# Kernel optimization log

Measured on AMD Instinct MI355X. Metric: run time of the kernel, lower is better.

The kernel has to match this reference:

```python
import jax, jax.numpy as jnp
import numpy as np
from jax import lax

K = 7            # cfg.network.PSROI_BINS == pool_size
FEAT_STRIDE = 16
LAMDA = 0.1
D_PER_BIN = 8    # feature channels per position-sensitive bin -> C = K*K*8 = 392


def _bilinear(feat, y, x, extra_idx):
    """Bilinearly sample feat[H,W,...] at float coords (y,x); extra_idx are
    integer index arrays (broadcast to y.shape) selecting trailing feat axes."""
    H, W = feat.shape[0], feat.shape[1]
    y0f = jnp.floor(y); x0f = jnp.floor(x)
    wy = (y - y0f)[..., None]
    wx = (x - x0f)[..., None]
    y0 = jnp.clip(y0f.astype(jnp.int32), 0, H - 1)
    y1 = jnp.clip(y0f.astype(jnp.int32) + 1, 0, H - 1)
    x0 = jnp.clip(x0f.astype(jnp.int32), 0, W - 1)
    x1 = jnp.clip(x0f.astype(jnp.int32) + 1, 0, W - 1)
    def g(yi, xi):
        return feat[(yi, xi) + extra_idx]
    return ((1 - wy) * (1 - wx) * g(y0, x0) + (1 - wy) * wx * g(y0, x1)
            + wy * (1 - wx) * g(y1, x0) + wy * wx * g(y1, x1))


def ps_roi(f, rois, k, feat_stride, offsets=None):
    """Position-sensitive RoI pooling. f: [H,W,C] with C = k*k*D (bin-major
    channel layout). rois: [N,5] (batch, x1, y1, x2, y2) in image coords.
    offsets (optional): [N, k*k, G, 2] per-bin, per-channel-group (x,y) shifts
    in image coords. Returns [N, D, k, k]."""
    H, W, C = f.shape
    N = rois.shape[0]
    kk = k * k
    D = C // kk
    x1 = rois[:, 1] / feat_stride
    y1 = rois[:, 2] / feat_stride
    x2 = (rois[:, 3] + 1.0) / feat_stride
    y2 = (rois[:, 4] + 1.0) / feat_stride
    bw = (x2 - x1) / k  # [N]
    bh = (y2 - y1) / k
    jj = jnp.tile(jnp.arange(k, dtype=f.dtype), k)     # bin = i*k + j
    ii = jnp.repeat(jnp.arange(k, dtype=f.dtype), k)
    cx = x1[:, None] + (jj + 0.5) * bw[:, None]        # [N, kk] bin centers
    cy = y1[:, None] + (ii + 0.5) * bh[:, None]
    bins = jnp.arange(kk, dtype=jnp.int32)
    if offsets is None:
        feat = f.reshape(H, W, kk, D)
        b = jnp.broadcast_to(bins, (N, kk))
        vals = _bilinear(feat, cy, cx, (b,))           # [N, kk, D]
    else:
        G = offsets.shape[2]
        cxg = cx[:, :, None] + offsets[..., 0] / feat_stride  # [N, kk, G]
        cyg = cy[:, :, None] + offsets[..., 1] / feat_stride
        feat = f.reshape(H, W, kk, G, D // G)
        b = jnp.broadcast_to(bins[None, :, None], (N, kk, G))
        g = jnp.broadcast_to(jnp.arange(G, dtype=jnp.int32)[None, None, :], (N, kk, G))
        vals = _bilinear(feat, cyg, cxg, (b, g))       # [N, kk, G, D//G]
        vals = vals.reshape(N, kk, D)
    return jnp.transpose(vals.reshape(N, k, k, D), (0, 3, 1, 2))  # [N, D, k, k]


def setup_inputs():
    key = jax.random.key(0)
    kf, kw, k1, k2 = jax.random.split(key, 4)
    H = W = 128
    C = K * K * D_PER_BIN
    N = 2048
    features = jax.random.normal(kf, (1, H, W, C), jnp.float32)
    conv_w = jax.random.normal(kw, (3, 3, C, 2 * 4 * K * K), jnp.float32) * 0.01
    img = float(H * FEAT_STRIDE)
    xy1 = jax.random.uniform(k1, (N, 2), minval=0.0, maxval=img * 0.6)
    wh = jax.random.uniform(k2, (N, 2), minval=32.0, maxval=img * 0.4)
    xy2 = jnp.minimum(xy1 + wh, img - 1.0)
    rois = jnp.concatenate([jnp.zeros((N, 1)), xy1[:, :1], xy1[:, 1:], xy2[:, :1], xy2[:, 1:]], axis=1).astype(jnp.float32)
    return {"features": features, "rois": rois, "conv_w": conv_w}


def reference(features, rois, conv_w):
    # offset branch: 3x3 conv (no bias) -> PS-RoI pool -> scale by lamda*roi size
    offset_map = lax.conv_general_dilated(features, conv_w, (1, 1), 'SAME',
                                          dimension_numbers=('NHWC', 'HWIO', 'NHWC'))
    off = ps_roi(offset_map[0], rois, K, FEAT_STRIDE)          # [N, 8, K, K]
    N = off.shape[0]
    off = off.reshape(N, -1, 2, K, K)                          # [N, 4, 2, K, K]
    off = jnp.transpose(off, (2, 3, 4, 1, 0))                  # [2, K, K, 4, N]
    roi_w = rois[:, 3] - rois[:, 1] + 1.0
    roi_h = rois[:, 4] - rois[:, 2] + 1.0
    off = jnp.stack((off[0] * roi_w * LAMDA, off[1] * roi_h * LAMDA), axis=0)
    off = jnp.transpose(off, (4, 1, 2, 3, 0))                  # [N, K, K, 4, 2]
    off = off.reshape(N, K * K, -1, 2)                         # [N, kk, 4, 2]
    # deformable PS-RoI pooling of the features with predicted offsets
    return ps_roi(features[0], rois, K, FEAT_STRIDE, offsets=off)  # [N, 8, K, K]
```

## Files before the change

### kernel.cpp

```cpp
#include <hip/hip_runtime.h>
#include <hip/hip_cooperative_groups.h>
#include <cstddef>
#include <cstdint>

namespace cg = cooperative_groups;

#define HH    128
#define WW    128
#define CC    392
#define NPIX  (HH*WW)
#define NROI  2048
#define PSK   7
#define NBIN  49
#define LAMDA 0.1f

#define CPAD      448
#define HPAD      130
#define NPADCO    512
#define SEGSTRIDE (9*CPAD)
#define BKK       64
#define NQ        63

#define NBLK    1024
#define NTHR    256
#define GSTRIDE (NBLK*NTHR)
#define FTOT    (HPAD*HPAD*(CPAD/8))
#define WTILES  (9*14*16)
#define POOLTOT (NROI*NBIN*4)

typedef _Float16 half8   __attribute__((ext_vector_type(8)));
typedef _Float16 half2v  __attribute__((ext_vector_type(2)));
typedef float    floatx4 __attribute__((ext_vector_type(4)));

__device__ __forceinline__ void async_ld16(const _Float16* g, _Float16* l) {
  __builtin_amdgcn_global_load_lds((const __attribute__((address_space(1))) void*)g,
                                   (__attribute__((address_space(3))) void*)l,
                                   16, 0, 0);
}

__device__ __forceinline__ void prep_features(const float* __restrict__ F,
                                              _Float16* __restrict__ Fh,
                                              int gtid, int stride) {
  for (int idx = gtid; idx < FTOT; idx += stride) {
    const int p  = idx / (CPAD / 8);
    const int cgi = idx - p * (CPAD / 8);
    const int c  = cgi * 8;
    const int py = p / HPAD;
    const int px = p - py * HPAD;
    half8 h;
#pragma unroll
    for (int i = 0; i < 8; ++i) h[i] = (_Float16)0.f;
    if (py >= 1 && py <= HH && px >= 1 && px <= WW && c < CC) {
      const float* src = F + ((size_t)(py - 1) * WW + (px - 1)) * CC + c;
      const float4 v0 = *(const float4*)src;
      const float4 v1 = *(const float4*)(src + 4);
      h[0] = (_Float16)v0.x; h[1] = (_Float16)v0.y;
      h[2] = (_Float16)v0.z; h[3] = (_Float16)v0.w;
      h[4] = (_Float16)v1.x; h[5] = (_Float16)v1.y;
      h[6] = (_Float16)v1.z; h[7] = (_Float16)v1.w;
    }
    *(half8*)(Fh + (size_t)p * CPAD + c) = h;
  }
}

__device__ __forceinline__ void prep_weights(const float* __restrict__ Wt,
                                             _Float16* __restrict__ Bth,
                                             float (*tile)[33],
                                             int bid, int t, int nblocks) {
  for (int tl = bid; tl < WTILES; tl += nblocks) {
    const int seg = tl / (14 * 16);
    const int rem = tl - seg * (14 * 16);
    const int cit = rem / 16;
    const int cot = rem - cit * 16;
    const int ci0 = cit * 32, co0 = cot * 32;
    __syncthreads();
#pragma unroll
    for (int i = 0; i < 4; ++i) {
      const int idx = t + i * 256;
      const int lr = idx >> 5;
      const int lc = idx & 31;
      const int ci = ci0 + lr, co = co0 + lc;
      float v = 0.f;
      if (ci < CC && co < CC) v = Wt[((size_t)seg * CC + ci) * CC + co];
      tile[lr][lc] = v;
    }
    __syncthreads();
#pragma unroll
    for (int i = 0; i < 4; ++i) {
      const int idx = t + i * 256;
      const int lr = idx >> 5;
      const int lc = idx & 31;
      Bth[(size_t)(co0 + lr) * SEGSTRIDE + seg * CPAD + ci0 + lc] = (_Float16)tile[lc][lr];
    }
  }
}

__device__ __forceinline__ void conv_phase(const _Float16* __restrict__ Fh,
                                           const _Float16* __restrict__ Bth,
                                           _Float16* __restrict__ OM,
                                           _Float16* As, _Float16* Bs,
                                           int cb, int t) {
  const int L = t & 63;
  const int w = t >> 6;
  const int row0 = (cb & 127) * 128;
  const int col0 = (cb >> 7) * 128;

  const int srow = L >> 3;
  const int kofs = ((L & 7) ^ srow) * 8;

  const int ya = row0 >> 7;
  const int nbase = col0 + w * 32 + srow;

  const int wm = (w >> 1) * 64;
  const int wn = (w & 1) * 64;
  const int fr = L & 15;
  const int quad = L >> 4;
  const int pg0 = (quad ^ (fr & 7)) * 8;
  const int pg1 = ((4 + quad) ^ (fr & 7)) * 8;

  floatx4 acc[4][4];
#pragma unroll
  for (int i = 0; i < 4; ++i)
#pragma unroll
    for (int j = 0; j < 4; ++j) {
      floatx4 z = {0.f, 0.f, 0.f, 0.f};
      acc[i][j] = z;
    }

  for (int q = 0; q < NQ; ++q) {
    const int seg = q / 7;
    const int it  = q - seg * 7;
    const int dy = seg / 3 - 1;
    const int dx = seg - (seg / 3) * 3 - 1;
    const int fy = ya + 1 + dy;
    const int cbofs = it * BKK;
    const _Float16* gArow = Fh + ((size_t)fy * HPAD + (1 + dx)) * CPAD + kofs + cbofs;
    const _Float16* gB = Bth + (size_t)nbase * SEGSTRIDE + seg * CPAD + kofs + cbofs;

#pragma unroll
    for (int j = 0; j < 4; ++j) {
      const int xr = w * 32 + j * 8 + srow;
      async_ld16(gArow + (size_t)xr * CPAD, &As[(w * 32 + j * 8) * BKK]);
    }
#pragma unroll
    for (int j = 0; j < 4; ++j) {
      async_ld16(gB + (size_t)(j * 8) * SEGSTRIDE, &Bs[(w * 32 + j * 8) * BKK]);
    }
    __syncthreads();

    half8 a0[4], a1[4], b0[4], b1[4];
#pragma unroll
    for (int mt = 0; mt < 4; ++mt) {
      const int rb = (wm + mt * 16 + fr) * BKK;
      a0[mt] = *(const half8*)(&As[rb + pg0]);
      a1[mt] = *(const half8*)(&As[rb + pg1]);
    }
#pragma unroll
    for (int nt = 0; nt < 4; ++nt) {
      const int rb = (wn + nt * 16 + fr) * BKK;
      b0[nt] = *(const half8*)(&Bs[rb + pg0]);
      b1[nt] = *(const half8*)(&Bs[rb + pg1]);
    }
#pragma unroll
    for (int mt = 0; mt < 4; ++mt)
#pragma unroll
      for (int nt = 0; nt < 4; ++nt)
        acc[mt][nt] = __builtin_amdgcn_mfma_f32_16x16x32_f16(a0[mt], b0[nt], acc[mt][nt], 0, 0, 0);
#pragma unroll
    for (int mt = 0; mt < 4; ++mt)
#pragma unroll
      for (int nt = 0; nt < 4; ++nt)
        acc[mt][nt] = __builtin_amdgcn_mfma_f32_16x16x32_f16(a1[mt], b1[nt], acc[mt][nt], 0, 0, 0);
    __syncthreads();
  }

#pragma unroll
  for (int mt = 0; mt < 4; ++mt) {
    const int rbase = row0 + wm + mt * 16 + quad * 4;
#pragma unroll
    for (int nt = 0; nt < 4; ++nt) {
      const int col = col0 + wn + nt * 16 + fr;
      if (col < CC) {
#pragma unroll
        for (int r = 0; r < 4; ++r)
          OM[(size_t)(rbase + r) * CC + col] = (_Float16)acc[mt][nt][r];
      }
    }
  }
}

__device__ __forceinline__ void bilin_setup(float y, float x,
                                            int& iy0, int& iy1, int& ix0, int& ix1,
                                            float& w00, float& w01, float& w10, float& w11) {
  const float y0f = floorf(y), x0f = floorf(x);
  const float wy = y - y0f, wx = x - x0f;
  const int a = (int)y0f, b = (int)x0f;
  iy0 = min(max(a, 0), HH - 1);
  iy1 = min(max(a + 1, 0), HH - 1);
  ix0 = min(max(b, 0), WW - 1);
  ix1 = min(max(b + 1, 0), WW - 1);
  w00 = (1.f - wy) * (1.f - wx);
  w01 = (1.f - wy) * wx;
  w10 = wy * (1.f - wx);
  w11 = wy * wx;
}

__device__ __forceinline__ void pool_item(const _Float16* __restrict__ Fh,
                                          const float* __restrict__ R,
                                          const _Float16* __restrict__ OM,
                                          float* __restrict__ out, int tid) {
  const int g  = tid & 3;
  const int nb = tid >> 2;
  const int n  = nb / NBIN;
  const int b  = nb - n * NBIN;
  const int bi = b / PSK;
  const int bj = b - bi * PSK;

  const float rx1 = R[n * 5 + 1], ry1 = R[n * 5 + 2];
  const float rx2 = R[n * 5 + 3], ry2 = R[n * 5 + 4];
  const float x1 = rx1 * (1.f / 16.f);
  const float y1 = ry1 * (1.f / 16.f);
  const float x2 = (rx2 + 1.f) * (1.f / 16.f);
  const float y2 = (ry2 + 1.f) * (1.f / 16.f);
  const float bw = (x2 - x1) * (1.f / 7.f);
  const float bh = (y2 - y1) * (1.f / 7.f);
  const float cx = x1 + ((float)bj + 0.5f) * bw;
  const float cy = y1 + ((float)bi + 0.5f) * bh;
  const float sxs = (rx2 - rx1 + 1.f) * (LAMDA / 16.f);
  const float sys = (ry2 - ry1 + 1.f) * (LAMDA / 16.f);

  int iy0, iy1, ix0, ix1;
  float w00, w01, w10, w11;
  bilin_setup(cy, cx, iy0, iy1, ix0, ix1, w00, w01, w10, w11);

  const size_t c0 = (size_t)b * 8 + 2 * g;
  const half2v m00 = *(const half2v*)(OM + (size_t)(iy0 * WW + ix0) * CC + c0);
  const half2v m01 = *(const half2v*)(OM + (size_t)(iy0 * WW + ix1) * CC + c0);
  const half2v m10 = *(const half2v*)(OM + (size_t)(iy1 * WW + ix0) * CC + c0);
  const half2v m11 = *(const half2v*)(OM + (size_t)(iy1 * WW + ix1) * CC + c0);

  const float ox = w00 * (float)m00[0] + w01 * (float)m01[0]
                 + w10 * (float)m10[0] + w11 * (float)m11[0];
  const float oy = w00 * (float)m00[1] + w01 * (float)m01[1]
                 + w10 * (float)m10[1] + w11 * (float)m11[1];

  const float sx = cx + ox * sxs;
  const float sy = cy + oy * sys;

  int jy0, jy1, jx0, jx1;
  float u00, u01, u10, u11;
  bilin_setup(sy, sx, jy0, jy1, jx0, jx1, u00, u01, u10, u11);

  const half2v q00 = *(const half2v*)(Fh + ((size_t)(jy0 + 1) * HPAD + (jx0 + 1)) * CPAD + c0);
  const half2v q01 = *(const half2v*)(Fh + ((size_t)(jy0 + 1) * HPAD + (jx1 + 1)) * CPAD + c0);
  const half2v q10 = *(const half2v*)(Fh + ((size_t)(jy1 + 1) * HPAD + (jx0 + 1)) * CPAD + c0);
  const half2v q11 = *(const half2v*)(Fh + ((size_t)(jy1 + 1) * HPAD + (jx1 + 1)) * CPAD + c0);

  const float v0 = u00 * (float)q00[0] + u01 * (float)q01[0]
                 + u10 * (float)q10[0] + u11 * (float)q11[0];
  const float v1 = u00 * (float)q00[1] + u01 * (float)q01[1]
                 + u10 * (float)q10[1] + u11 * (float)q11[1];

  out[((size_t)n * 8 + 2 * g + 0) * NBIN + b] = v0;
  out[((size_t)n * 8 + 2 * g + 1) * NBIN + b] = v1;
}

__global__ __launch_bounds__(NTHR, 4)
void mega_kernel(const float* __restrict__ F, const float* __restrict__ R,
                 const float* __restrict__ Wt, _Float16* __restrict__ OM,
                 _Float16* __restrict__ Fh, _Float16* __restrict__ Bth,
                 float* __restrict__ out) {
  __shared__ __align__(16) _Float16 smem[2 * 128 * BKK];
  const int bid = blockIdx.x;
  const int t = threadIdx.x;
  const int gtid = bid * NTHR + t;
  cg::grid_group grid = cg::this_grid();

  prep_features(F, Fh, gtid, GSTRIDE);
  prep_weights(Wt, Bth, (float(*)[33])smem, bid, t, NBLK);

  __threadfence();
  grid.sync();

  if (bid < 512)
    conv_phase(Fh, Bth, OM, smem, smem + 128 * BKK, bid, t);

  __threadfence();
  grid.sync();

  for (int item = gtid; item < POOLTOT; item += GSTRIDE)
    pool_item(Fh, R, OM, out, item);
}

__global__ __launch_bounds__(256)
void prep_kernel_sa(const float* __restrict__ F, const float* __restrict__ Wt,
                    _Float16* __restrict__ Fh, _Float16* __restrict__ Bth) {
  __shared__ float tile[32][33];
  const int bid = blockIdx.x;
  const int t = threadIdx.x;
  prep_features(F, Fh, bid * 256 + t, gridDim.x * 256);
  prep_weights(Wt, Bth, tile, bid, t, gridDim.x);
}

__global__ __launch_bounds__(256, 4)
void conv_kernel_sa(const _Float16* __restrict__ Fh, const _Float16* __restrict__ Bth,
                    _Float16* __restrict__ OM) {
  __shared__ __align__(16) _Float16 smem[2 * 128 * BKK];
  conv_phase(Fh, Bth, OM, smem, smem + 128 * BKK, blockIdx.x, threadIdx.x);
}

__global__ __launch_bounds__(256)
void pool_kernel_sa(const _Float16* __restrict__ Fh, const float* __restrict__ R,
                    const _Float16* __restrict__ OM, float* __restrict__ out) {
  const int tid = blockIdx.x * 256 + threadIdx.x;
  if (tid < POOLTOT) pool_item(Fh, R, OM, out, tid);
}

extern "C" void kernel_launch(void* const* d_in, const int* in_sizes, int n_in,
                              void* d_out, int out_size, void* d_ws, size_t ws_size,
                              hipStream_t stream) {
  const float* F  = (const float*)d_in[0];
  const float* R  = (const float*)d_in[1];
  const float* Wt = (const float*)d_in[2];
  float* out = (float*)d_out;

  const size_t omBytes  = (size_t)NPIX * CC * sizeof(_Float16);
  const size_t fhBytes  = (size_t)HPAD * HPAD * CPAD * sizeof(_Float16);

  _Float16* OM  = (_Float16*)d_ws;
  _Float16* Fh  = (_Float16*)((char*)d_ws + omBytes);
  _Float16* Bth = (_Float16*)((char*)d_ws + omBytes + fhBytes);

  int maxBlk = 0;
  hipError_t qerr = hipOccupancyMaxActiveBlocksPerMultiprocessor(&maxBlk, mega_kernel, NTHR, 0);
  bool tryCoop = (qerr == hipSuccess && maxBlk >= 4);

  if (tryCoop) {
    void* args[] = {(void*)&F, (void*)&R, (void*)&Wt, (void*)&OM,
                    (void*)&Fh, (void*)&Bth, (void*)&out};
    hipError_t err = hipLaunchCooperativeKernel((const void*)mega_kernel,
                                                dim3(NBLK), dim3(NTHR),
                                                args, 0, stream);
    if (err == hipSuccess) return;
    (void)hipGetLastError();
  }

  prep_kernel_sa<<<2048, 256, 0, stream>>>(F, Wt, Fh, Bth);
  conv_kernel_sa<<<512, 256, 0, stream>>>(Fh, Bth, OM);
  pool_kernel_sa<<<(POOLTOT + 255) / 256, 256, 0, stream>>>(Fh, R, OM, out);
}
```

Baseline: 165.9 us.

## Split conv K-dimension across two partial outputs and use thin tile for tail columns

The conv GEMM work is reshaped. The 392 output columns are covered by three 128-wide tiles plus a thin 16-wide tile instead of four 128-wide tiles, which avoids computing padded columns. The K loop is split in two halves written to separate partial buffers, so all 1024 blocks get work instead of 512. Pooling moves to a separate kernel launch. It sums the two partials while bilinearly sampling, with each lane loading one corner and combining results through shuffles. This trades more workspace and double offset-map reads for better load balance and fewer wasted MMAs.

```diff
diff --git a/kernel.cpp b/kernel.cpp
--- a/kernel.cpp
+++ b/kernel.cpp
@@ -16,7 +16,7 @@
 
 #define CPAD      448
 #define HPAD      130
-#define NPADCO    512
+#define NPADCO    416
 #define SEGSTRIDE (9*CPAD)
 #define BKK       64
 #define NQ        63
@@ -25,7 +25,7 @@
 #define NTHR    256
 #define GSTRIDE (NBLK*NTHR)
 #define FTOT    (HPAD*HPAD*(CPAD/8))
-#define WTILES  (9*14*16)
+#define WTILES  (9*14*13)
 #define POOLTOT (NROI*NBIN*4)
 
 typedef _Float16 half8   __attribute__((ext_vector_type(8)));
@@ -42,11 +42,11 @@
                                               _Float16* __restrict__ Fh,
                                               int gtid, int stride) {
   for (int idx = gtid; idx < FTOT; idx += stride) {
-    const int p  = idx / (CPAD / 8);
+    const int p   = idx / (CPAD / 8);
     const int cgi = idx - p * (CPAD / 8);
-    const int c  = cgi * 8;
-    const int py = p / HPAD;
-    const int px = p - py * HPAD;
+    const int c   = cgi * 8;
+    const int py  = p / HPAD;
+    const int px  = p - py * HPAD;
     half8 h;
 #pragma unroll
     for (int i = 0; i < 8; ++i) h[i] = (_Float16)0.f;
@@ -68,10 +68,10 @@
                                              float (*tile)[33],
                                              int bid, int t, int nblocks) {
   for (int tl = bid; tl < WTILES; tl += nblocks) {
-    const int seg = tl / (14 * 16);
-    const int rem = tl - seg * (14 * 16);
-    const int cit = rem / 16;
-    const int cot = rem - cit * 16;
+    const int seg = tl / (14 * 13);
+    const int rem = tl - seg * (14 * 13);
+    const int cit = rem / 13;
+    const int cot = rem - cit * 13;
     const int ci0 = cit * 32, co0 = cot * 32;
     __syncthreads();
 #pragma unroll
@@ -95,19 +95,16 @@
   }
 }
 
-__device__ __forceinline__ void conv_phase(const _Float16* __restrict__ Fh,
-                                           const _Float16* __restrict__ Bth,
-                                           _Float16* __restrict__ OM,
-                                           _Float16* As, _Float16* Bs,
-                                           int cb, int t) {
+__device__ __forceinline__ void conv_fat(const _Float16* __restrict__ Fh,
+                                         const _Float16* __restrict__ Bth,
+                                         _Float16* __restrict__ OMp,
+                                         _Float16* As, _Float16* Bs,
+                                         int row0, int col0, int q0, int q1, int t) {
   const int L = t & 63;
   const int w = t >> 6;
-  const int row0 = (cb & 127) * 128;
-  const int col0 = (cb >> 7) * 128;
 
   const int srow = L >> 3;
   const int kofs = ((L & 7) ^ srow) * 8;
-
   const int ya = row0 >> 7;
   const int nbase = col0 + w * 32 + srow;
 
@@ -127,15 +124,15 @@
       acc[i][j] = z;
     }
 
-  for (int q = 0; q < NQ; ++q) {
+  for (int q = q0; q < q1; ++q) {
     const int seg = q / 7;
     const int it  = q - seg * 7;
     const int dy = seg / 3 - 1;
     const int dx = seg - (seg / 3) * 3 - 1;
     const int fy = ya + 1 + dy;
-    const int cbofs = it * BKK;
-    const _Float16* gArow = Fh + ((size_t)fy * HPAD + (1 + dx)) * CPAD + kofs + cbofs;
-    const _Float16* gB = Bth + (size_t)nbase * SEGSTRIDE + seg * CPAD + kofs + cbofs;
+    const int cb = it * BKK;
+    const _Float16* gArow = Fh + ((size_t)fy * HPAD + (1 + dx)) * CPAD + kofs + cb;
+    const _Float16* gB = Bth + (size_t)nbase * SEGSTRIDE + seg * CPAD + kofs + cb;
 
 #pragma unroll
     for (int j = 0; j < 4; ++j) {
@@ -143,9 +140,8 @@
       async_ld16(gArow + (size_t)xr * CPAD, &As[(w * 32 + j * 8) * BKK]);
     }
 #pragma unroll
-    for (int j = 0; j < 4; ++j) {
+    for (int j = 0; j < 4; ++j)
       async_ld16(gB + (size_t)(j * 8) * SEGSTRIDE, &Bs[(w * 32 + j * 8) * BKK]);
-    }
     __syncthreads();
 
     half8 a0[4], a1[4], b0[4], b1[4];
@@ -183,10 +179,102 @@
       if (col < CC) {
 #pragma unroll
         for (int r = 0; r < 4; ++r)
-          OM[(size_t)(rbase + r) * CC + col] = (_Float16)acc[mt][nt][r];
+          OMp[(size_t)(rbase + r) * CC + col] = (_Float16)acc[mt][nt][r];
       }
     }
   }
+}
+
+__device__ __forceinline__ void conv_thin(const _Float16* __restrict__ Fh,
+                                          const _Float16* __restrict__ Bth,
+                                          _Float16* __restrict__ OMp,
+                                          _Float16* As, _Float16* Bs,
+                                          int row0, int q0, int q1, int t) {
+  const int L = t & 63;
+  const int w = t >> 6;
+
+  const int srow = L >> 3;
+  const int kofs = ((L & 7) ^ srow) * 8;
+  const int ya = row0 >> 7;
+  const int nbase = 384 + w * 8 + srow;
+
+  const int wm = w * 32;
+  const int fr = L & 15;
+  const int quad = L >> 4;
+  const int pg0 = (quad ^ (fr & 7)) * 8;
+  const int pg1 = ((4 + quad) ^ (fr & 7)) * 8;
+
+  floatx4 acc[2];
+#pragma unroll
+  for (int i = 0; i < 2; ++i) {
+    floatx4 z = {0.f, 0.f, 0.f, 0.f};
+    acc[i] = z;
+  }
+
+  for (int q = q0; q < q1; ++q) {
+    const int seg = q / 7;
+    const int it  = q - seg * 7;
+    const int dy = seg / 3 - 1;
+    const int dx = seg - (seg / 3) * 3 - 1;
+    const int fy = ya + 1 + dy;
+    const int cb = it * BKK;
+    const _Float16* gArow = Fh + ((size_t)fy * HPAD + (1 + dx)) * CPAD + kofs + cb;
+
+#pragma unroll
+    for (int j = 0; j < 4; ++j) {
+      const int xr = w * 32 + j * 8 + srow;
+      async_ld16(gArow + (size_t)xr * CPAD, &As[(w * 32 + j * 8) * BKK]);
+    }
+    if (w < 2) {
+      const _Float16* gB = Bth + (size_t)nbase * SEGSTRIDE + seg * CPAD + kofs + cb;
+      async_ld16(gB, &Bs[(w * 8) * BKK]);
+    }
+    __syncthreads();
+
+    half8 a0[2], a1[2];
+#pragma unroll
+    for (int mt = 0; mt < 2; ++mt) {
+      const int rb = (wm + mt * 16 + fr) * BKK;
+      a0[mt] = *(const half8*)(&As[rb + pg0]);
+      a1[mt] = *(const half8*)(&As[rb + pg1]);
+    }
+    const half8 b0 = *(const half8*)(&Bs[fr * BKK + pg0]);
+    const half8 b1 = *(const half8*)(&Bs[fr * BKK + pg1]);
+#pragma unroll
+    for (int mt = 0; mt < 2; ++mt)
+      acc[mt] = __builtin_amdgcn_mfma_f32_16x16x32_f16(a0[mt], b0, acc[mt], 0, 0, 0);
+#pragma unroll
+    for (int mt = 0; mt < 2; ++mt)
+      acc[mt] = __builtin_amdgcn_mfma_f32_16x16x32_f16(a1[mt], b1, acc[mt], 0, 0, 0);
+    __syncthreads();
+  }
+
+#pragma unroll
+  for (int mt = 0; mt < 2; ++mt) {
+    const int rbase = row0 + wm + mt * 16 + quad * 4;
+    const int col = 384 + fr;
+    if (col < CC) {
+#pragma unroll
+      for (int r = 0; r < 4; ++r)
+        OMp[(size_t)(rbase + r) * CC + col] = (_Float16)acc[mt][r];
+    }
+  }
+}
+
+__device__ __forceinline__ void conv_dispatch(const _Float16* Fh, const _Float16* Bth,
+                                              _Float16* OMa, _Float16* OMb,
+                                              _Float16* As, _Float16* Bs,
+                                              int bid, int t) {
+  const int x = bid & 127;
+  const int rest = bid >> 7;
+  const int kz = (rest < 6) ? (rest / 3) : (rest - 6);
+  _Float16* OMp = kz ? OMb : OMa;
+  const int q0 = kz * 32;
+  const int q1 = kz ? NQ : 32;
+  if (rest < 6)
+    conv_fat(Fh, Bth, OMp, As, Bs, x * 128, (rest % 3) * 128, q0, q1, t);
+  else
+    conv_thin(Fh, Bth, OMp, As, Bs, x * 128, q0, q1, t);
 }
 
 __device__ __forceinline__ void bilin_setup(float y, float x,
@@ -207,9 +295,10 @@
 
 __device__ __forceinline__ void pool_item(const _Float16* __restrict__ Fh,
                                           const float* __restrict__ R,
-                                          const _Float16* __restrict__ OM,
+                                          const _Float16* __restrict__ OMa,
+                                          const _Float16* __restrict__ OMb,
                                           float* __restrict__ out, int tid) {
-  const int g  = tid & 3;
+  const int q  = tid & 3;
   const int nb = tid >> 2;
   const int n  = nb / NBIN;
   const int b  = nb - n * NBIN;
@@ -233,24 +322,31 @@
   float w00, w01, w10, w11;
   bilin_setup(cy, cx, iy0, iy1, ix0, ix1, w00, w01, w10, w11);
 
-  const size_t c0 = (size_t)b * 8 + 2 * g;
-  const half2v m00 = *(const half2v*)(OM + (size_t)(iy0 * WW + ix0) * CC + c0);
-  const half2v m01 = *(const half2v*)(OM + (size_t)(iy0 * WW + ix1) * CC + c0);
-  const half2v m10 = *(const half2v*)(OM + (size_t)(iy1 * WW + ix0) * CC + c0);
-  const half2v m11 = *(const half2v*)(OM + (size_t)(iy1 * WW + ix1) * CC + c0);
-
-  const float ox = w00 * (float)m00[0] + w01 * (float)m01[0]
-                 + w10 * (float)m10[0] + w11 * (float)m11[0];
-  const float oy = w00 * (float)m00[1] + w01 * (float)m01[1]
-                 + w10 * (float)m10[1] + w11 * (float)m11[1];
-
-  const float sx = cx + ox * sxs;
-  const float sy = cy + oy * sys;
+  const int cyi = (q >> 1) ? iy1 : iy0;
+  const int cxi = (q & 1) ? ix1 : ix0;
+  const float wq = (q == 0) ? w00 : (q == 1) ? w01 : (q == 2) ? w10 : w11;
+
+  const size_t base = (size_t)(cyi * WW + cxi) * CC + (size_t)b * 8;
+  const half8 ha = *(const half8*)(OMa + base);
+  const half8 hb = *(const half8*)(OMb + base);
+
+  float o8[8];
+#pragma unroll
+  for (int i = 0; i < 8; ++i)
+    o8[i] = wq * ((float)ha[i] + (float)hb[i]);
+#pragma unroll
+  for (int i = 0; i < 8; ++i) o8[i] += __shfl_xor(o8[i], 1);
+#pragma unroll
+  for (int i = 0; i < 8; ++i) o8[i] += __shfl_xor(o8[i], 2);
+
+  const float sx = cx + o8[2 * q] * sxs;
+  const float sy = cy + o8[2 * q + 1] * sys;
 
   int jy0, jy1, jx0, jx1;
   float u00, u01, u10, u11;
   bilin_setup(sy, sx, jy0, jy1, jx0, jx1, u00, u01, u10, u11);
 
+  const size_t c0 = (size_t)b * 8 + 2 * q;
   const half2v q00 = *(const half2v*)(Fh + ((size_t)(jy0 + 1) * HPAD + (jx0 + 1)) * CPAD + c0);
   const half2v q01 = *(const half2v*)(Fh + ((size_t)(jy0 + 1) * HPAD + (jx1 + 1)) * CPAD + c0);
   const half2v q10 = *(const half2v*)(Fh + ((size_t)(jy1 + 1) * HPAD + (jx0 + 1)) * CPAD + c0);
@@ -261,59 +357,48 @@
   const float v1 = u00 * (float)q00[1] + u01 * (float)q01[1]
                  + u10 * (float)q10[1] + u11 * (float)q11[1];
 
-  out[((size_t)n * 8 + 2 * g + 0) * NBIN + b] = v0;
-  out[((size_t)n * 8 + 2 * g + 1) * NBIN + b] = v1;
+  out[((size_t)n * 8 + 2 * q + 0) * NBIN + b] = v0;
+  out[((size_t)n * 8 + 2 * q + 1) * NBIN + b] = v1;
 }
 
 __global__ __launch_bounds__(NTHR, 4)
-void mega_kernel(const float* __restrict__ F, const float* __restrict__ R,
-                 const float* __restrict__ Wt, _Float16* __restrict__ OM,
-                 _Float16* __restrict__ Fh, _Float16* __restrict__ Bth,
-                 float* __restrict__ out) {
+void mega_kernel(const float* __restrict__ F, const float* __restrict__ Wt,
+                 _Float16* __restrict__ OMa, _Float16* __restrict__ OMb,
+                 _Float16* __restrict__ Fh, _Float16* __restrict__ Bth) {
   __shared__ __align__(16) _Float16 smem[2 * 128 * BKK];
   const int bid = blockIdx.x;
   const int t = threadIdx.x;
-  const int gtid = bid * NTHR + t;
   cg::grid_group grid = cg::this_grid();
 
-  prep_features(F, Fh, gtid, GSTRIDE);
+  prep_features(F, Fh, bid * NTHR + t, GSTRIDE);
   prep_weights(Wt, Bth, (float(*)[33])smem, bid, t, NBLK);
 
   __threadfence();
   grid.sync();
 
-  if (bid < 512)
-    conv_phase(Fh, Bth, OM, smem, smem + 128 * BKK, bid, t);
-
-  __threadfence();
-  grid.sync();
-
-  for (int item = gtid; item < POOLTOT; item += GSTRIDE)
-    pool_item(Fh, R, OM, out, item);
+  conv_dispatch(Fh, Bth, OMa, OMb, smem, smem + 128 * BKK, bid, t);
+}
+
+__global__ __launch_bounds__(256)
+void pool_kernel(const _Float16* __restrict__ Fh, const float* __restrict__ R,
+                 const _Float16* __restrict__ OMa, const _Float16* __restrict__ OMb,
+                 float* __restrict__ out) {
+  pool_item(Fh, R, OMa, OMb, out, blockIdx.x * 256 + threadIdx.x);
 }
 
 __global__ __launch_bounds__(256)
 void prep_kernel_sa(const float* __restrict__ F, const float* __restrict__ Wt,
                     _Float16* __restrict__ Fh, _Float16* __restrict__ Bth) {
   __shared__ float tile[32][33];
-  const int bid = blockIdx.x;
-  const int t = threadIdx.x;
-  prep_features(F, Fh, bid * 256 + t, gridDim.x * 256);
-  prep_weights(Wt, Bth, tile, bid, t, gridDim.x);
+  prep_features(F, Fh, blockIdx.x * 256 + threadIdx.x, gridDim.x * 256);
+  prep_weights(Wt, Bth, tile, blockIdx.x, threadIdx.x, gridDim.x);
 }
 
 __global__ __launch_bounds__(256, 4)
 void conv_kernel_sa(const _Float16* __restrict__ Fh, const _Float16* __restrict__ Bth,
-                    _Float16* __restrict__ OM) {
+                    _Float16* __restrict__ OMa, _Float16* __restrict__ OMb) {
   __shared__ __align__(16) _Float16 smem[2 * 128 * BKK];
-  conv_phase(Fh, Bth, OM, smem, smem + 128 * BKK, blockIdx.x, threadIdx.x);
-}
-
-__global__ __launch_bounds__(256)
-void pool_kernel_sa(const _Float16* __restrict__ Fh, const float* __restrict__ R,
-                    const _Float16* __restrict__ OM, float* __restrict__ out) {
-  const int tid = blockIdx.x * 256 + threadIdx.x;
-  if (tid < POOLTOT) pool_item(Fh, R, OM, out, tid);
+  conv_dispatch(Fh, Bth, OMa, OMb, smem, smem + 128 * BKK, blockIdx.x, threadIdx.x);
 }
 
 extern "C" void kernel_launch(void* const* d_in, const int* in_sizes, int n_in,
@@ -327,25 +412,30 @@
   const size_t omBytes  = (size_t)NPIX * CC * sizeof(_Float16);
   const size_t fhBytes  = (size_t)HPAD * HPAD * CPAD * sizeof(_Float16);
 
-  _Float16* OM  = (_Float16*)d_ws;
-  _Float16* Fh  = (_Float16*)((char*)d_ws + omBytes);
-  _Float16* Bth = (_Float16*)((char*)d_ws + omBytes + fhBytes);
+  _Float16* OMa = (_Float16*)d_ws;
+  _Float16* OMb = OMa + (size_t)NPIX * CC;
+  _Float16* Fh  = (_Float16*)((char*)d_ws + 2 * omBytes);
+  _Float16* Bth = (_Float16*)((char*)d_ws + 2 * omBytes + fhBytes);
 
   int maxBlk = 0;
   hipError_t qerr = hipOccupancyMaxActiveBlocksPerMultiprocessor(&maxBlk, mega_kernel, NTHR, 0);
-  bool tryCoop = (qerr == hipSuccess && maxBlk >= 4);
-
-  if (tryCoop) {
-    void* args[] = {(void*)&F, (void*)&R, (void*)&Wt, (void*)&OM,
-                    (void*)&Fh, (void*)&Bth, (void*)&out};
+  bool coopOk = (qerr == hipSuccess && maxBlk >= 4);
+
+  if (coopOk) {
+    void* args[] = {(void*)&F, (void*)&Wt, (void*)&OMa, (void*)&OMb,
+                    (void*)&Fh, (void*)&Bth};
     hipError_t err = hipLaunchCooperativeKernel((const void*)mega_kernel,
                                                 dim3(NBLK), dim3(NTHR),
                                                 args, 0, stream);
-    if (err == hipSuccess) return;
-    (void)hipGetLastError();
-  }
-
-  prep_kernel_sa<<<2048, 256, 0, stream>>>(F, Wt, Fh, Bth);
-  conv_kernel_sa<<<512, 256, 0, stream>>>(Fh, Bth, OM);
-  pool_kernel_sa<<<(POOLTOT + 255) / 256, 256, 0, stream>>>(Fh, R, OM, out);
-}
+    if (err != hipSuccess) {
+      (void)hipGetLastError();
+      coopOk = false;
+    }
+  }
+  if (!coopOk) {
+    prep_kernel_sa<<<2048, 256, 0, stream>>>(F, Wt, Fh, Bth);
+    conv_kernel_sa<<<NBLK, 256, 0, stream>>>(Fh, Bth, OMa, OMb);
+  }
+
+  pool_kernel<<<POOLTOT / 256, 256, 0, stream>>>(Fh, R, OMa, OMb, out);
+}
```

New measurement: 158.3 us. 1.05x faster.
